# Kernel tuning notes

Measured on AMD Instinct MI355X. Metric: run time of the kernel, lower is better.

## Reference

```python
import jax, jax.numpy as jnp
import numpy as np

CODE_NUM = 100000
GRAPH = 256
HIDDEN = 256
TIME = 256


def gru_cell(x, h, w_ih, w_hh, b_ih, b_hh):
    # torch.nn.GRUCell math. x:[N,G] h:[N,H] w_ih:[3H,G] w_hh:[3H,H]
    gi = x @ w_ih.T + b_ih
    gh = h @ w_hh.T + b_hh
    i_r, i_z, i_n = jnp.split(gi, 3, axis=-1)
    h_r, h_z, h_n = jnp.split(gh, 3, axis=-1)
    r = jax.nn.sigmoid(i_r + h_r)
    z = jax.nn.sigmoid(i_z + h_z)
    n = jnp.tanh(i_n + r * h_n)
    return (1.0 - z) * n + z * h


def setup_inputs() -> dict:
    key = jax.random.key(0)
    ks = jax.random.split(key, 12)
    s_ih = 1.0 / np.sqrt(HIDDEN)
    return {
        "interval": jax.random.uniform(ks[0], (1,), jnp.float32) * 100.0 + 1.0,
        "t": 0,
        "co_embeddings": jax.random.normal(ks[1], (CODE_NUM, GRAPH), jnp.float32),
        "divided": jax.random.randint(ks[2], (CODE_NUM, 3), 0, 2, jnp.int32),
        "no_embeddings": jax.random.normal(ks[3], (1, GRAPH), jnp.float32),
        "unrelated_embeddings": jax.random.normal(ks[4], (1, GRAPH), jnp.float32),
        "is_last": 0,
        "hidden_state": jax.random.normal(ks[5], (CODE_NUM, HIDDEN), jnp.float32),
        "weight_ih": jax.random.uniform(ks[6], (3 * HIDDEN, GRAPH), jnp.float32, -s_ih, s_ih),
        "weight_hh": jax.random.uniform(ks[7], (3 * HIDDEN, HIDDEN), jnp.float32, -s_ih, s_ih),
        "bias_ih": jax.random.uniform(ks[8], (3 * HIDDEN,), jnp.float32, -s_ih, s_ih),
        "bias_hh": jax.random.uniform(ks[9], (3 * HIDDEN,), jnp.float32, -s_ih, s_ih),
        "time_w": jax.random.normal(ks[10], (TIME, 1), jnp.float32) * 0.02,
        "time_b": jax.random.normal(ks[11], (TIME,), jnp.float32) * 0.02,
    }


def reference(interval, t, co_embeddings, divided, no_embeddings,
              unrelated_embeddings, is_last, hidden_state,
              weight_ih, weight_hh, bias_ih, bias_hh, time_w, time_b):
    # time branch: tanh(Linear(1/log(interval + e)))
    inv = 1.0 / jnp.log(interval[:, None] + jnp.exp(jnp.float32(1.0)))  # [1,1]
    time_features = jnp.tanh(inv @ time_w.T + time_b)                  # [1,TIME]

    # not is_last branch: gather rows where any of divided[:,0:3] > 0,
    # run GRUCell, scatter into zeros, max-reduce over selected rows.
    # Masked formulation is row-wise exact (GRUCell acts per row).
    mask = jnp.any(divided > 0, axis=1)                                 # [N]
    h_all = gru_cell(co_embeddings, hidden_state,
                     weight_ih, weight_hh, bias_ih, bias_hh)            # [N,H]
    h_new = jnp.where(mask[:, None], h_all, 0.0)                        # scatter into zeros
    output = jnp.max(jnp.where(mask[:, None], h_all, -jnp.inf), axis=0) # max over gathered rows, [H]
    return output + time_features, h_new
```

## Files before the change

kernel.cpp:

```cpp
#include <hip/hip_runtime.h>
#include <hip/hip_bf16.h>
#include <math.h>

#define M_ROWS 100000
#define NGROUPS 3125
#define NTILES_TOTAL 391
#define TILES_PER_XCD 49
#define ROWS_PER_XCD 12500
#define NTILES 49
#define NCHUNK 49152

typedef __attribute__((ext_vector_type(8)))  short  short8;
typedef __attribute__((ext_vector_type(16))) float  float16v;

__device__ __forceinline__ unsigned short bf16_rne(float f) {
    unsigned u = __builtin_bit_cast(unsigned, f);
    u += 0x7FFFu + ((u >> 16) & 1u);
    return (unsigned short)(u >> 16);
}

__device__ __forceinline__ float sigmoid_fast(float x) {
    return 1.0f / (1.0f + __expf(-x));
}
__device__ __forceinline__ float tanh_fast(float x) {
    return 1.0f - 2.0f / (__expf(2.0f * x) + 1.0f);
}

__device__ __forceinline__ unsigned pack2_rn(float lo, float hi) {
    __hip_bfloat162 t = __float22bfloat162_rn(float2{lo, hi});
    unsigned u;
    __builtin_memcpy(&u, &t, 4);
    return u;
}

__device__ __forceinline__ short8 pack_bf16x8(float4 a, float4 b) {
    union { short8 s; unsigned u[4]; } r;
    r.u[0] = pack2_rn(a.x, a.y);
    r.u[1] = pack2_rn(a.z, a.w);
    r.u[2] = pack2_rn(b.x, b.y);
    r.u[3] = pack2_rn(b.z, b.w);
    return r.s;
}

__global__ void prep_kernel(const float* __restrict__ X,
                            const float* __restrict__ H,
                            const float* __restrict__ wih,
                            const float* __restrict__ whh,
                            const int* __restrict__ divided,
                            unsigned short* __restrict__ wswz,
                            unsigned short* __restrict__ apack,
                            unsigned int* __restrict__ maxacc,
                            int* __restrict__ maskbuf,
                            unsigned int* __restrict__ donecnt,
                            int pack_blocks)
{
    const int b   = blockIdx.x;
    const int tid = threadIdx.x;

    if (b < pack_blocks) {
        int gt   = b * 256 + tid;
        int lane = gt & 63;
        int u    = gt >> 6;
        int gr   = u >> 4;
        int kc   = u & 15;
        int row  = gr * 32 + (lane & 31);
        int col  = kc * 16 + (lane >> 5) * 8;
        const float* xs = X + (size_t)row * 256 + col;
        const float* hs = H + (size_t)row * 256 + col;
        float4 a = reinterpret_cast<const float4*>(xs)[0];
        float4 c = reinterpret_cast<const float4*>(xs)[1];
        reinterpret_cast<short8*>(apack)[(size_t)(u * 2) * 64 + lane] = pack_bf16x8(a, c);
        float4 d = reinterpret_cast<const float4*>(hs)[0];
        float4 e = reinterpret_cast<const float4*>(hs)[1];
        reinterpret_cast<short8*>(apack)[(size_t)(u * 2 + 1) * 64 + lane] = pack_bf16x8(d, e);
        return;
    }

    int bb = b - pack_blocks;
    if (bb < 192) {
        int idx  = bb * 256 + tid;
        int lane = idx & 63;
        int t    = idx >> 6;
        int s    = t % 6;
        int t2   = t / 6;
        int kc   = t2 & 15;
        int g    = t2 >> 4;
        int row  = (s % 3) * 256 + g * 32 + (lane & 31);
        int col  = kc * 16 + (lane >> 5) * 8;
        const float* src = (s < 3 ? wih : whh) + row * 256 + col;
        float4 a = reinterpret_cast<const float4*>(src)[0];
        float4 c = reinterpret_cast<const float4*>(src)[1];
        uint4 p;
        p.x = (unsigned)bf16_rne(a.x) | ((unsigned)bf16_rne(a.y) << 16);
        p.y = (unsigned)bf16_rne(a.z) | ((unsigned)bf16_rne(a.w) << 16);
        p.z = (unsigned)bf16_rne(c.x) | ((unsigned)bf16_rne(c.y) << 16);
        p.w = (unsigned)bf16_rne(c.z) | ((unsigned)bf16_rne(c.w) << 16);
        reinterpret_cast<uint4*>(wswz)[idx] = p;
    } else if (bb < 192 + 391) {
        int m = (bb - 192) * 256 + tid;
        if (m < M_ROWS)
            maskbuf[m] = (divided[3 * m] > 0) | (divided[3 * m + 1] > 0) | (divided[3 * m + 2] > 0);
    } else {
        maxacc[tid] = 0u;
        if (tid == 0) *donecnt = 0u;
    }
}

__global__ __launch_bounds__(512, 2) void gru_main_packed(
    const unsigned short* __restrict__ Apack,
    const float* __restrict__ H,
    const unsigned short* __restrict__ Wswz,
    const float* __restrict__ bih,
    const float* __restrict__ bhh,
    const int* __restrict__ maskbuf,
    const float* __restrict__ interval,
    const float* __restrict__ time_w,
    const float* __restrict__ time_b,
    float* __restrict__ hnew,
    unsigned int* __restrict__ maxacc,
    unsigned int* __restrict__ donecnt,
    float* __restrict__ out)
{
    __shared__ unsigned short Wlds[49152];
    __shared__ int islast;

    const int tid  = threadIdx.x;
    const int lane = tid & 63;
    const int wave = tid >> 6;
    const int l32  = lane & 31;
    const int hi   = lane >> 5;

    const int b    = blockIdx.x;
    const int xcd  = b & 7;
    const int slot = b >> 3;
    const int g    = slot & 7;
    const int sub  = slot >> 3;

    const int tbeg = xcd * TILES_PER_XCD + sub;
    const int tend = min(xcd * TILES_PER_XCD + TILES_PER_XCD, NTILES_TOTAL);

    {
        const uint4* ws = reinterpret_cast<const uint4*>(Wswz) + (size_t)g * 6144;
        uint4* wd = reinterpret_cast<uint4*>(Wlds);
        #pragma unroll
        for (int i = 0; i < 12; ++i) wd[i * 512 + tid] = ws[i * 512 + tid];
    }
    __syncthreads();

    const short8* wbase = reinterpret_cast<const short8*>(Wlds);
    const short8* A8b   = reinterpret_cast<const short8*>(Apack);
    const int jj = g * 32 + l32;
    const float bir = bih[jj], biz = bih[256 + jj], bin_ = bih[512 + jj];
    const float bhr = bhh[jj], bhz = bhh[256 + jj], bhn  = bhh[512 + jj];

    float colmax = -__builtin_inff();

    for (int t = tbeg; t < tend; t += 4) {
        const int wrow0 = t * 256 + wave * 32;
        if (wrow0 >= M_ROWS) continue;
        const int gr0 = wrow0 >> 5;
        const short8* A8 = A8b + (size_t)gr0 * 2048 + lane;

        float16v acc[6];
        #pragma unroll
        for (int s = 0; s < 6; ++s)
            #pragma unroll
            for (int q = 0; q < 16; ++q) acc[s][q] = 0.0f;

        short8 bx[4], bh[4];
        #pragma unroll
        for (int p = 0; p < 4; ++p) {
            bx[p] = A8[p * 128];
            bh[p] = A8[p * 128 + 64];
        }

        #pragma unroll
        for (int kc = 0; kc < 16; ++kc) {
            const int cur = kc & 3;
            const short8 ax = bx[cur];
            const short8 ah = bh[cur];
            if (kc < 12) {
                bx[cur] = A8[(kc + 4) * 128];
                bh[cur] = A8[(kc + 4) * 128 + 64];
            }
            const short8* wk = wbase + kc * 384 + lane;
            acc[0] = __builtin_amdgcn_mfma_f32_32x32x16_bf16(ax, wk[0],   acc[0], 0, 0, 0);
            acc[1] = __builtin_amdgcn_mfma_f32_32x32x16_bf16(ax, wk[64],  acc[1], 0, 0, 0);
            acc[2] = __builtin_amdgcn_mfma_f32_32x32x16_bf16(ax, wk[128], acc[2], 0, 0, 0);
            acc[3] = __builtin_amdgcn_mfma_f32_32x32x16_bf16(ah, wk[192], acc[3], 0, 0, 0);
            acc[4] = __builtin_amdgcn_mfma_f32_32x32x16_bf16(ah, wk[256], acc[4], 0, 0, 0);
            acc[5] = __builtin_amdgcn_mfma_f32_32x32x16_bf16(ah, wk[320], acc[5], 0, 0, 0);
        }

        #pragma unroll
        for (int reg = 0; reg < 16; ++reg) {
            const int rl = (reg & 3) + 8 * (reg >> 2) + 4 * hi;
            const int m  = wrow0 + rl;
            float gir = acc[0][reg] + bir;
            float giz = acc[1][reg] + biz;
            float gin = acc[2][reg] + bin_;
            float ghr = acc[3][reg] + bhr;
            float ghz = acc[4][reg] + bhz;
            float ghn = acc[5][reg] + bhn;
            float r = sigmoid_fast(gir + ghr);
            float z = sigmoid_fast(giz + ghz);
            float n = tanh_fast(gin + r * ghn);
            float hp = H[(size_t)m * 256 + jj];
            float hv = (1.0f - z) * n + z * hp;
            int mk = maskbuf[m];
            __builtin_nontemporal_store(mk ? hv : 0.0f, &hnew[(size_t)m * 256 + jj]);
            if (mk) colmax = fmaxf(colmax, hv);
        }
    }

    colmax = fmaxf(colmax, __shfl_xor(colmax, 32));
    if (hi == 0) {
        unsigned bb = __builtin_bit_cast(unsigned, colmax);
        unsigned u  = (bb & 0x80000000u) ? ~bb : (bb | 0x80000000u);
        atomicMax(&maxacc[jj], u);
    }

    __syncthreads();
    if (tid == 0) {
        __threadfence();
        islast = (atomicAdd(donecnt, 1u) == 255u) ? 1 : 0;
    }
    __syncthreads();
    if (islast && tid < 256) {
        unsigned u  = atomicMax(&maxacc[tid], 0u);
        unsigned bb2 = (u & 0x80000000u) ? (u & 0x7FFFFFFFu) : ~u;
        float mx  = __builtin_bit_cast(float, bb2);
        float inv = 1.0f / logf(interval[0] + 2.718281828459045f);
        out[tid]  = mx + tanhf(inv * time_w[tid] + time_b[tid]);
    }
}

__global__ __launch_bounds__(512, 2) void gru_main_legacy(
    const float* __restrict__ X,
    const float* __restrict__ H,
    const unsigned short* __restrict__ Wswz,
    const float* __restrict__ bih,
    const float* __restrict__ bhh,
    const int* __restrict__ maskbuf,
    float* __restrict__ hnew,
    unsigned int* __restrict__ maxacc)
{
    __shared__ unsigned short Wlds[NCHUNK];

    const int tid  = threadIdx.x;
    const int lane = tid & 63;
    const int wave = tid >> 6;
    const int l32  = lane & 31;
    const int hi   = lane >> 5;

    const int b    = blockIdx.x;
    const int xcd  = b & 7;
    const int slot = b >> 3;
    const int g    = slot & 7;
    const int sub  = slot >> 3;
    const int base  = xcd * ROWS_PER_XCD;
    const int limit = base + ROWS_PER_XCD;

    {
        const uint4* ws = reinterpret_cast<const uint4*>(Wswz) + (size_t)g * 6144;
        uint4* wd = reinterpret_cast<uint4*>(Wlds);
        #pragma unroll
        for (int i = 0; i < 12; ++i) wd[i * 512 + tid] = ws[i * 512 + tid];
    }
    __syncthreads();

    const short8* wbase = reinterpret_cast<const short8*>(Wlds);
    const int jj = g * 32 + l32;
    const float bir = bih[jj], biz = bih[256 + jj], bin_ = bih[512 + jj];
    const float bhr = bhh[jj], bhz = bhh[256 + jj], bhn  = bhh[512 + jj];

    float colmax = -__builtin_inff();

    for (int t = sub; t < NTILES; t += 4) {
        const int wrow0 = base + t * 256 + wave * 32;
        if (wrow0 >= limit) continue;
        const int arow = min(wrow0 + l32, limit - 1);
        const float4* X4 = reinterpret_cast<const float4*>(X) + (size_t)arow * 64;
        const float4* H4 = reinterpret_cast<const float4*>(H) + (size_t)arow * 64;

        float16v acc[6];
        #pragma unroll
        for (int s = 0; s < 6; ++s)
            #pragma unroll
            for (int q = 0; q < 16; ++q) acc[s][q] = 0.0f;

        float4 xb[2][4], hb[2][4];
        #pragma unroll
        for (int c = 0; c < 2; ++c)
            #pragma unroll
            for (int f = 0; f < 2; ++f) {
                int fi = c * 4 + hi * 2 + f;
                xb[0][c * 2 + f] = X4[fi];
                hb[0][c * 2 + f] = H4[fi];
            }

        #pragma unroll
        for (int q = 0; q < 8; ++q) {
            const int cur = q & 1, nxt = cur ^ 1;
            if (q < 7) {
                #pragma unroll
                for (int c = 0; c < 2; ++c)
                    #pragma unroll
                    for (int f = 0; f < 2; ++f) {
                        int fi = (q * 2 + 2 + c) * 4 + hi * 2 + f;
                        xb[nxt][c * 2 + f] = X4[fi];
                        hb[nxt][c * 2 + f] = H4[fi];
                    }
            }
            short8 ax[2], ah[2];
            #pragma unroll
            for (int c = 0; c < 2; ++c) {
                ax[c] = pack_bf16x8(xb[cur][c * 2], xb[cur][c * 2 + 1]);
                ah[c] = pack_bf16x8(hb[cur][c * 2], hb[cur][c * 2 + 1]);
            }
            #pragma unroll
            for (int c = 0; c < 2; ++c) {
                const int kc = q * 2 + c;
                const short8* wk = wbase + (kc * 6) * 64 + lane;
                acc[0] = __builtin_amdgcn_mfma_f32_32x32x16_bf16(ax[c], wk[0],   acc[0], 0, 0, 0);
                acc[1] = __builtin_amdgcn_mfma_f32_32x32x16_bf16(ax[c], wk[64],  acc[1], 0, 0, 0);
                acc[2] = __builtin_amdgcn_mfma_f32_32x32x16_bf16(ax[c], wk[128], acc[2], 0, 0, 0);
                acc[3] = __builtin_amdgcn_mfma_f32_32x32x16_bf16(ah[c], wk[192], acc[3], 0, 0, 0);
                acc[4] = __builtin_amdgcn_mfma_f32_32x32x16_bf16(ah[c], wk[256], acc[4], 0, 0, 0);
                acc[5] = __builtin_amdgcn_mfma_f32_32x32x16_bf16(ah[c], wk[320], acc[5], 0, 0, 0);
            }
        }

        #pragma unroll
        for (int reg = 0; reg < 16; ++reg) {
            int rl = (reg & 3) + 8 * (reg >> 2) + 4 * hi;
            int m  = wrow0 + rl;
            if (m < limit) {
                float gir = acc[0][reg] + bir;
                float giz = acc[1][reg] + biz;
                float gin = acc[2][reg] + bin_;
                float ghr = acc[3][reg] + bhr;
                float ghz = acc[4][reg] + bhz;
                float ghn = acc[5][reg] + bhn;
                float r = sigmoid_fast(gir + ghr);
                float z = sigmoid_fast(giz + ghz);
                float n = tanh_fast(gin + r * ghn);
                float hp = H[(size_t)m * 256 + jj];
                float hv = (1.0f - z) * n + z * hp;
                int mk = maskbuf[m];
                __builtin_nontemporal_store(mk ? hv : 0.0f, &hnew[(size_t)m * 256 + jj]);
                if (mk) colmax = fmaxf(colmax, hv);
            }
        }
    }

    colmax = fmaxf(colmax, __shfl_xor(colmax, 32));
    if (hi == 0) {
        unsigned bb = __builtin_bit_cast(unsigned, colmax);
        unsigned u  = (bb & 0x80000000u) ? ~bb : (bb | 0x80000000u);
        atomicMax(&maxacc[jj], u);
    }
}

__global__ void finalize_kernel(const unsigned int* __restrict__ maxacc,
                                const float* __restrict__ interval,
                                const float* __restrict__ time_w,
                                const float* __restrict__ time_b,
                                float* __restrict__ out)
{
    int j = threadIdx.x;
    unsigned u = maxacc[j];
    unsigned b = (u & 0x80000000u) ? (u & 0x7FFFFFFFu) : ~u;
    float mx = __builtin_bit_cast(float, b);
    float inv = 1.0f / logf(interval[0] + 2.718281828459045f);
    out[j] = mx + tanhf(inv * time_w[j] + time_b[j]);
}

extern "C" void kernel_launch(void* const* d_in, const int* in_sizes, int n_in,
                              void* d_out, int out_size, void* d_ws, size_t ws_size,
                              hipStream_t stream) {
    const float* interval = (const float*)d_in[0];
    const float* co       = (const float*)d_in[2];
    const int*   divided  = (const int*)d_in[3];
    const float* hidden   = (const float*)d_in[7];
    const float* wih      = (const float*)d_in[8];
    const float* whh      = (const float*)d_in[9];
    const float* bih      = (const float*)d_in[10];
    const float* bhh      = (const float*)d_in[11];
    const float* time_w   = (const float*)d_in[12];
    const float* time_b   = (const float*)d_in[13];

    float* out  = (float*)d_out;
    float* hnew = out + 256;

    unsigned short* wswz    = (unsigned short*)d_ws;
    unsigned int*   maxacc  = (unsigned int*)((char*)d_ws + 786432);
    int*            maskbuf = (int*)((char*)d_ws + 787456);
    unsigned int*   donecnt = (unsigned int*)((char*)d_ws + 1187456);
    unsigned short* apack   = (unsigned short*)((char*)d_ws + 2097152);

    const size_t NEED = 2097152ull + 102400000ull;
    const bool packed = (ws_size >= NEED);
    const int pb = packed ? 12500 : 0;

    prep_kernel<<<pb + 584, 256, 0, stream>>>(co, hidden, wih, whh, divided,
                                              wswz, apack, maxacc, maskbuf,
                                              donecnt, pb);

    if (packed) {
        gru_main_packed<<<256, 512, 0, stream>>>(apack, hidden, wswz, bih, bhh,
                                                 maskbuf, interval, time_w, time_b,
                                                 hnew, maxacc, donecnt, out);
    } else {
        gru_main_legacy<<<256, 512, 0, stream>>>(co, hidden, wswz,
                                                 bih, bhh, maskbuf, hnew, maxacc);
        finalize_kernel<<<1, 256, 0, stream>>>(maxacc, interval, time_w, time_b, out);
    }
}
```

Before: 459.0 us.

## Process two row groups per wave with register-cached weights and cross-tile prefetch

Each wave now computes two 32-row groups per iteration, so each weight fragment loaded from LDS feeds two MFMAs. Weight fragments are double-buffered in registers, and A-operand loads for the next tile are prefetched during the current tile's K loop. Work is split into 512-row super-tiles balanced across XCDs. The aim is to halve LDS weight traffic per MFMA and hide global load latency between tiles. The cost is many more accumulator and operand registers, which can lower occupancy or cause spills.

Result: slower. 522.2 us (+13.8%).

```diff
diff --git a/kernel.cpp b/kernel.cpp
--- a/kernel.cpp
+++ b/kernel.cpp
@@ -4,8 +4,7 @@
 
 #define M_ROWS 100000
 #define NGROUPS 3125
-#define NTILES_TOTAL 391
-#define TILES_PER_XCD 49
+#define NSUPER 196
 #define ROWS_PER_XCD 12500
 #define NTILES 49
 #define NCHUNK 49152
@@ -136,8 +135,8 @@
     const int g    = slot & 7;
     const int sub  = slot >> 3;
 
-    const int tbeg = xcd * TILES_PER_XCD + sub;
-    const int tend = min(xcd * TILES_PER_XCD + TILES_PER_XCD, NTILES_TOTAL);
+    const int sbeg = xcd * 24 + (xcd < 4 ? xcd : 4);
+    const int send = sbeg + (xcd < 4 ? 25 : 24);
 
     {
         const uint4* ws = reinterpret_cast<const uint4*>(Wswz) + (size_t)g * 6144;
@@ -155,61 +154,105 @@
 
     float colmax = -__builtin_inff();
 
-    for (int t = tbeg; t < tend; t += 4) {
-        const int wrow0 = t * 256 + wave * 32;
-        if (wrow0 >= M_ROWS) continue;
-        const int gr0 = wrow0 >> 5;
-        const short8* A8 = A8b + (size_t)gr0 * 2048 + lane;
-
-        float16v acc[6];
-        #pragma unroll
-        for (int s = 0; s < 6; ++s)
+    short8 wr[2][6];
+    #pragma unroll
+    for (int s = 0; s < 6; ++s) wr[0][s] = wbase[s * 64 + lane];
+
+    short8 bx0[4], bh0[4], bx1[4], bh1[4];
+    const int T0 = sbeg + sub;
+    {
+        int gp0 = T0 * 16 + 2 * wave; if (gp0 > NGROUPS - 1) gp0 = NGROUPS - 1;
+        int gp1 = gp0 + 1;            if (gp1 > NGROUPS - 1) gp1 = NGROUPS - 1;
+        const short8* P0 = A8b + (size_t)gp0 * 2048 + lane;
+        const short8* P1 = A8b + (size_t)gp1 * 2048 + lane;
+        #pragma unroll
+        for (int p = 0; p < 4; ++p) {
+            bx0[p] = P0[p * 128]; bh0[p] = P0[p * 128 + 64];
+            bx1[p] = P1[p * 128]; bh1[p] = P1[p * 128 + 64];
+        }
+    }
+
+    for (int T = T0; T < send; T += 4) {
+        const int gr0 = T * 16 + 2 * wave;
+        if (gr0 >= NGROUPS) continue;
+        const int gr1 = gr0 + 1;
+        const bool v1 = (gr1 < NGROUPS);
+
+        const short8* A0c = A8b + (size_t)gr0 * 2048 + lane;
+        const short8* A1c = A8b + (size_t)(v1 ? gr1 : gr0) * 2048 + lane;
+
+        int Tn = T + 4; if (Tn >= send) Tn = T;
+        int ng0 = Tn * 16 + 2 * wave; if (ng0 >= NGROUPS) ng0 = gr0;
+        int ng1 = ng0 + 1;            if (ng1 >= NGROUPS) ng1 = ng0;
+        const short8* A0n = A8b + (size_t)ng0 * 2048 + lane;
+        const short8* A1n = A8b + (size_t)ng1 * 2048 + lane;
+
+        float16v acc[12];
+        #pragma unroll
+        for (int s = 0; s < 12; ++s)
             #pragma unroll
             for (int q = 0; q < 16; ++q) acc[s][q] = 0.0f;
 
-        short8 bx[4], bh[4];
-        #pragma unroll
-        for (int p = 0; p < 4; ++p) {
-            bx[p] = A8[p * 128];
-            bh[p] = A8[p * 128 + 64];
+        #pragma unroll
+        for (int kc = 0; kc < 16; ++kc) {
+            const int sl = kc & 3;
+            const short8 ax0 = bx0[sl], ah0 = bh0[sl];
+            const short8 ax1 = bx1[sl], ah1 = bh1[sl];
+
+            {
+                const int kr = kc + 4;
+                const short8* P0 = (kr < 16) ? A0c : A0n;
+                const short8* P1 = (kr < 16) ? A1c : A1n;
+                const int ko = (kr < 16) ? kr : (kr - 16);
+                bx0[sl] = P0[ko * 128]; bh0[sl] = P0[ko * 128 + 64];
+                bx1[sl] = P1[ko * 128]; bh1[sl] = P1[ko * 128 + 64];
+            }
+
+            const int cb = kc & 1;
+            {
+                const int kn = (kc + 1) & 15;
+                const short8* wn = wbase + kn * 384 + lane;
+                #pragma unroll
+                for (int s = 0; s < 6; ++s) wr[cb ^ 1][s] = wn[s * 64];
+            }
+
+            acc[0]  = __builtin_amdgcn_mfma_f32_32x32x16_bf16(ax0, wr[cb][0], acc[0],  0, 0, 0);
+            acc[6]  = __builtin_amdgcn_mfma_f32_32x32x16_bf16(ax1, wr[cb][0], acc[6],  0, 0, 0);
+            acc[1]  = __builtin_amdgcn_mfma_f32_32x32x16_bf16(ax0, wr[cb][1], acc[1],  0, 0, 0);
+            acc[7]  = __builtin_amdgcn_mfma_f32_32x32x16_bf16(ax1, wr[cb][1], acc[7],  0, 0, 0);
+            acc[2]  = __builtin_amdgcn_mfma_f32_32x32x16_bf16(ax0, wr[cb][2], acc[2],  0, 0, 0);
+            acc[8]  = __builtin_amdgcn_mfma_f32_32x32x16_bf16(ax1, wr[cb][2], acc[8],  0, 0, 0);
+            acc[3]  = __builtin_amdgcn_mfma_f32_32x32x16_bf16(ah0, wr[cb][3], acc[3],  0, 0, 0);
+            acc[9]  = __builtin_amdgcn_mfma_f32_32x32x16_bf16(ah1, wr[cb][3], acc[9],  0, 0, 0);
+            acc[4]  = __builtin_amdgcn_mfma_f32_32x32x16_bf16(ah0, wr[cb][4], acc[4],  0, 0, 0);
+            acc[10] = __builtin_amdgcn_mfma_f32_32x32x16_bf16(ah1, wr[cb][4], acc[10], 0, 0, 0);
+            acc[5]  = __builtin_amdgcn_mfma_f32_32x32x16_bf16(ah0, wr[cb][5], acc[5],  0, 0, 0);
+            acc[11] = __builtin_amdgcn_mfma_f32_32x32x16_bf16(ah1, wr[cb][5], acc[11], 0, 0, 0);
         }
 
         #pragma unroll
-        for (int kc = 0; kc < 16; ++kc) {
-            const int cur = kc & 3;
-            const short8 ax = bx[cur];
-            const short8 ah = bh[cur];
-            if (kc < 12) {
-                bx[cur] = A8[(kc + 4) * 128];
-                bh[cur] = A8[(kc + 4) * 128 + 64];
-            }
-            const short8* wk = wbase + kc * 384 + lane;
-            acc[0] = __builtin_amdgcn_mfma_f32_32x32x16_bf16(ax, wk[0],   acc[0], 0, 0, 0);
-            acc[1] = __builtin_amdgcn_mfma_f32_32x32x16_bf16(ax, wk[64],  acc[1], 0, 0, 0);
-            acc[2] = __builtin_amdgcn_mfma_f32_32x32x16_bf16(ax, wk[128], acc[2], 0, 0, 0);
-            acc[3] = __builtin_amdgcn_mfma_f32_32x32x16_bf16(ah, wk[192], acc[3], 0, 0, 0);
-            acc[4] = __builtin_amdgcn_mfma_f32_32x32x16_bf16(ah, wk[256], acc[4], 0, 0, 0);
-            acc[5] = __builtin_amdgcn_mfma_f32_32x32x16_bf16(ah, wk[320], acc[5], 0, 0, 0);
-        }
-
-        #pragma unroll
-        for (int reg = 0; reg < 16; ++reg) {
-            const int rl = (reg & 3) + 8 * (reg >> 2) + 4 * hi;
-            const int m  = wrow0 + rl;
-            float gir = acc[0][reg] + bir;
-            float giz = acc[1][reg] + biz;
-            float gin = acc[2][reg] + bin_;
-            float ghr = acc[3][reg] + bhr;
-            float ghz = acc[4][reg] + bhz;
-            float ghn = acc[5][reg] + bhn;
-            float r = sigmoid_fast(gir + ghr);
-            float z = sigmoid_fast(giz + ghz);
-            float n = tanh_fast(gin + r * ghn);
-            float hp = H[(size_t)m * 256 + jj];
-            float hv = (1.0f - z) * n + z * hp;
-            int mk = maskbuf[m];
-            __builtin_nontemporal_store(mk ? hv : 0.0f, &hnew[(size_t)m * 256 + jj]);
-            if (mk) colmax = fmaxf(colmax, hv);
+        for (int grp = 0; grp < 2; ++grp) {
+            if (grp == 1 && !v1) continue;
+            const int mb = (grp ? gr1 : gr0) * 32;
+            #pragma unroll
+            for (int reg = 0; reg < 16; ++reg) {
+                const int rl = (reg & 3) + 8 * (reg >> 2) + 4 * hi;
+                const int m  = mb + rl;
+                float gir = acc[grp * 6 + 0][reg] + bir;
+                float giz = acc[grp * 6 + 1][reg] + biz;
+                float gin = acc[grp * 6 + 2][reg] + bin_;
+                float ghr = acc[grp * 6 + 3][reg] + bhr;
+                float ghz = acc[grp * 6 + 4][reg] + bhz;
+                float ghn = acc[grp * 6 + 5][reg] + bhn;
+                float r = sigmoid_fast(gir + ghr);
+                float z = sigmoid_fast(giz + ghz);
+                float n = tanh_fast(gin + r * ghn);
+                float hp = H[(size_t)m * 256 + jj];
+                float hv = (1.0f - z) * n + z * hp;
+                int mk = maskbuf[m];
+                __builtin_nontemporal_store(mk ? hv : 0.0f, &hnew[(size_t)m * 256 + jj]);
+                if (mk) colmax = fmaxf(colmax, hv);
+            }
         }
     }
 
```

## Switch packed GRU path to 16x16x32 MFMA tiles with LDS-staged packing

Applied to the files above, without the earlier changes.

Changes the packed path from 32x32x16 to 16x16x32 bf16 MFMA. Weights are split into 16 column groups and the launch becomes 768 blocks of 256 threads, each wave looping over 16-row groups. The A operand for the next group is prefetched across iterations, and H and mask values are loaded before the matmul. The activation pack kernel now stages 32 rows through LDS so global reads and writes are coalesced. This targets occupancy, latency hiding and pack-kernel efficiency, at the cost of smaller MFMA tiles and three times as many blocks contending on the completion counter.

New measurement: 766.7 us. 67.0% more time.

```diff
diff --git a/kernel.cpp b/kernel.cpp
--- a/kernel.cpp
+++ b/kernel.cpp
@@ -3,14 +3,13 @@
 #include <math.h>
 
 #define M_ROWS 100000
-#define NGROUPS 3125
-#define NTILES_TOTAL 391
-#define TILES_PER_XCD 49
+#define NG16 6250
 #define ROWS_PER_XCD 12500
 #define NTILES 49
 #define NCHUNK 49152
 
 typedef __attribute__((ext_vector_type(8)))  short  short8;
+typedef __attribute__((ext_vector_type(4)))  float  float4v;
 typedef __attribute__((ext_vector_type(16))) float  float16v;
 
 __device__ __forceinline__ unsigned short bf16_rne(float f) {
@@ -52,27 +51,41 @@
                             unsigned int* __restrict__ maxacc,
                             int* __restrict__ maskbuf,
                             unsigned int* __restrict__ donecnt,
-                            int pack_blocks)
+                            int pack_blocks, int w16)
 {
+    __shared__ unsigned short slds[2][32][264];
+
     const int b   = blockIdx.x;
     const int tid = threadIdx.x;
 
     if (b < pack_blocks) {
-        int gt   = b * 256 + tid;
-        int lane = gt & 63;
-        int u    = gt >> 6;
-        int gr   = u >> 4;
-        int kc   = u & 15;
-        int row  = gr * 32 + (lane & 31);
-        int col  = kc * 16 + (lane >> 5) * 8;
-        const float* xs = X + (size_t)row * 256 + col;
-        const float* hs = H + (size_t)row * 256 + col;
-        float4 a = reinterpret_cast<const float4*>(xs)[0];
-        float4 c = reinterpret_cast<const float4*>(xs)[1];
-        reinterpret_cast<short8*>(apack)[(size_t)(u * 2) * 64 + lane] = pack_bf16x8(a, c);
-        float4 d = reinterpret_cast<const float4*>(hs)[0];
-        float4 e = reinterpret_cast<const float4*>(hs)[1];
-        reinterpret_cast<short8*>(apack)[(size_t)(u * 2 + 1) * 64 + lane] = pack_bf16x8(d, e);
+        const int r0 = b * 32;
+        #pragma unroll
+        for (int it = 0; it < 16; ++it) {
+            const int mat = it >> 3;
+            const int idx = (it & 7) * 256 + tid;
+            const int row = idx >> 6;
+            const int c4  = idx & 63;
+            const float* sp = (mat ? H : X) + (size_t)(r0 + row) * 256 + c4 * 4;
+            float4 v = *reinterpret_cast<const float4*>(sp);
+            uint2 w;
+            w.x = pack2_rn(v.x, v.y);
+            w.y = pack2_rn(v.z, v.w);
+            *reinterpret_cast<uint2*>(&slds[mat][row][c4 * 4]) = w;
+        }
+        __syncthreads();
+        #pragma unroll
+        for (int it = 0; it < 8; ++it) {
+            const int o    = it * 256 + tid;
+            const int gl   = o >> 10;
+            const int kc   = (o >> 7) & 7;
+            const int mat  = (o >> 6) & 1;
+            const int lane = o & 63;
+            const int rl   = gl * 16 + (lane & 15);
+            const int col  = kc * 32 + (lane >> 4) * 8;
+            short8 v = *reinterpret_cast<const short8*>(&slds[mat][rl][col]);
+            reinterpret_cast<short8*>(apack)[(size_t)b * 2048 + o] = v;
+        }
         return;
     }
 
@@ -83,11 +96,19 @@
         int t    = idx >> 6;
         int s    = t % 6;
         int t2   = t / 6;
-        int kc   = t2 & 15;
-        int g    = t2 >> 4;
-        int row  = (s % 3) * 256 + g * 32 + (lane & 31);
-        int col  = kc * 16 + (lane >> 5) * 8;
-        const float* src = (s < 3 ? wih : whh) + row * 256 + col;
+        int row, col;
+        if (w16) {
+            int kc  = t2 & 7;
+            int g16 = t2 >> 3;
+            row = (s % 3) * 256 + g16 * 16 + (lane & 15);
+            col = kc * 32 + (lane >> 4) * 8;
+        } else {
+            int kc = t2 & 15;
+            int g  = t2 >> 4;
+            row = (s % 3) * 256 + g * 32 + (lane & 31);
+            col = kc * 16 + (lane >> 5) * 8;
+        }
+        const float* src = (s < 3 ? wih : whh) + (size_t)row * 256 + col;
         float4 a = reinterpret_cast<const float4*>(src)[0];
         float4 c = reinterpret_cast<const float4*>(src)[1];
         uint4 p;
@@ -106,7 +127,7 @@
     }
 }
 
-__global__ __launch_bounds__(512, 2) void gru_main_packed(
+__global__ __launch_bounds__(256, 3) void gru_main16(
     const unsigned short* __restrict__ Apack,
     const float* __restrict__ H,
     const unsigned short* __restrict__ Wswz,
@@ -121,113 +142,116 @@
     unsigned int* __restrict__ donecnt,
     float* __restrict__ out)
 {
-    __shared__ unsigned short Wlds[49152];
+    __shared__ unsigned short Wlds[24576];
     __shared__ int islast;
 
     const int tid  = threadIdx.x;
     const int lane = tid & 63;
     const int wave = tid >> 6;
-    const int l32  = lane & 31;
-    const int hi   = lane >> 5;
+    const int l16  = lane & 15;
+    const int q    = lane >> 4;
 
     const int b    = blockIdx.x;
     const int xcd  = b & 7;
     const int slot = b >> 3;
-    const int g    = slot & 7;
-    const int sub  = slot >> 3;
-
-    const int tbeg = xcd * TILES_PER_XCD + sub;
-    const int tend = min(xcd * TILES_PER_XCD + TILES_PER_XCD, NTILES_TOTAL);
+    const int g16  = slot & 15;
+    const int sub  = slot >> 4;
+
+    const int gbeg = xcd * 781 + (xcd < 2 ? xcd : 2);
+    const int gend = gbeg + 781 + (xcd < 2 ? 1 : 0);
 
     {
-        const uint4* ws = reinterpret_cast<const uint4*>(Wswz) + (size_t)g * 6144;
+        const uint4* ws = reinterpret_cast<const uint4*>(Wswz) + (size_t)g16 * 3072;
         uint4* wd = reinterpret_cast<uint4*>(Wlds);
         #pragma unroll
-        for (int i = 0; i < 12; ++i) wd[i * 512 + tid] = ws[i * 512 + tid];
+        for (int i = 0; i < 12; ++i) wd[i * 256 + tid] = ws[i * 256 + tid];
     }
     __syncthreads();
 
     const short8* wbase = reinterpret_cast<const short8*>(Wlds);
     const short8* A8b   = reinterpret_cast<const short8*>(Apack);
-    const int jj = g * 32 + l32;
+    const int jj = g16 * 16 + l16;
     const float bir = bih[jj], biz = bih[256 + jj], bin_ = bih[512 + jj];
     const float bhr = bhh[jj], bhz = bhh[256 + jj], bhn  = bhh[512 + jj];
 
     float colmax = -__builtin_inff();
 
-    for (int t = tbeg; t < tend; t += 4) {
-        const int wrow0 = t * 256 + wave * 32;
-        if (wrow0 >= M_ROWS) continue;
-        const int gr0 = wrow0 >> 5;
-        const short8* A8 = A8b + (size_t)gr0 * 2048 + lane;
-
-        float16v acc[6];
-        #pragma unroll
-        for (int s = 0; s < 6; ++s)
-            #pragma unroll
-            for (int q = 0; q < 16; ++q) acc[s][q] = 0.0f;
-
+    int g0 = gbeg + sub * 4 + wave;
+    if (g0 < gend) {
+        const short8* A8 = A8b + (size_t)g0 * 1024 + lane;
         short8 bx[4], bh[4];
         #pragma unroll
-        for (int p = 0; p < 4; ++p) {
-            bx[p] = A8[p * 128];
-            bh[p] = A8[p * 128 + 64];
-        }
-
-        #pragma unroll
-        for (int kc = 0; kc < 16; ++kc) {
-            const int cur = kc & 3;
-            const short8 ax = bx[cur];
-            const short8 ah = bh[cur];
-            if (kc < 12) {
-                bx[cur] = A8[(kc + 4) * 128];
-                bh[cur] = A8[(kc + 4) * 128 + 64];
-            }
-            const short8* wk = wbase + kc * 384 + lane;
-            acc[0] = __builtin_amdgcn_mfma_f32_32x32x16_bf16(ax, wk[0],   acc[0], 0, 0, 0);
-            acc[1] = __builtin_amdgcn_mfma_f32_32x32x16_bf16(ax, wk[64],  acc[1], 0, 0, 0);
-            acc[2] = __builtin_amdgcn_mfma_f32_32x32x16_bf16(ax, wk[128], acc[2], 0, 0, 0);
-            acc[3] = __builtin_amdgcn_mfma_f32_32x32x16_bf16(ah, wk[192], acc[3], 0, 0, 0);
-            acc[4] = __builtin_amdgcn_mfma_f32_32x32x16_bf16(ah, wk[256], acc[4], 0, 0, 0);
-            acc[5] = __builtin_amdgcn_mfma_f32_32x32x16_bf16(ah, wk[320], acc[5], 0, 0, 0);
-        }
-
-        #pragma unroll
-        for (int reg = 0; reg < 16; ++reg) {
-            const int rl = (reg & 3) + 8 * (reg >> 2) + 4 * hi;
-            const int m  = wrow0 + rl;
-            float gir = acc[0][reg] + bir;
-            float giz = acc[1][reg] + biz;
-            float gin = acc[2][reg] + bin_;
-            float ghr = acc[3][reg] + bhr;
-            float ghz = acc[4][reg] + bhz;
-            float ghn = acc[5][reg] + bhn;
-            float r = sigmoid_fast(gir + ghr);
-            float z = sigmoid_fast(giz + ghz);
-            float n = tanh_fast(gin + r * ghn);
-            float hp = H[(size_t)m * 256 + jj];
-            float hv = (1.0f - z) * n + z * hp;
-            int mk = maskbuf[m];
-            __builtin_nontemporal_store(mk ? hv : 0.0f, &hnew[(size_t)m * 256 + jj]);
-            if (mk) colmax = fmaxf(colmax, hv);
-        }
-    }
-
+        for (int p = 0; p < 4; ++p) { bx[p] = A8[p * 128]; bh[p] = A8[p * 128 + 64]; }
+
+        for (int g = g0; g < gend; g += 24) {
+            A8 = A8b + (size_t)g * 1024 + lane;
+            int gn = g + 24; if (gn >= gend) gn = g;
+            const short8* An = A8b + (size_t)gn * 1024 + lane;
+
+            float hp[4]; int mk[4];
+            #pragma unroll
+            for (int r = 0; r < 4; ++r) {
+                const int m = g * 16 + q * 4 + r;
+                hp[r] = H[(size_t)m * 256 + jj];
+                mk[r] = maskbuf[m];
+            }
+
+            float4v acc[6];
+            #pragma unroll
+            for (int s = 0; s < 6; ++s)
+                #pragma unroll
+                for (int r = 0; r < 4; ++r) acc[s][r] = 0.0f;
+
+            #pragma unroll
+            for (int kc = 0; kc < 8; ++kc) {
+                const int sl = kc & 3;
+                const short8 ax = bx[sl], ah = bh[sl];
+                if (kc < 4) { bx[sl] = A8[(kc + 4) * 128]; bh[sl] = A8[(kc + 4) * 128 + 64]; }
+                else        { bx[sl] = An[(kc - 4) * 128]; bh[sl] = An[(kc - 4) * 128 + 64]; }
+                const short8* wk = wbase + kc * 384 + lane;
+                acc[0] = __builtin_amdgcn_mfma_f32_16x16x32_bf16(ax, wk[0],   acc[0], 0, 0, 0);
+                acc[1] = __builtin_amdgcn_mfma_f32_16x16x32_bf16(ax, wk[64],  acc[1], 0, 0, 0);
+                acc[2] = __builtin_amdgcn_mfma_f32_16x16x32_bf16(ax, wk[128], acc[2], 0, 0, 0);
+                acc[3] = __builtin_amdgcn_mfma_f32_16x16x32_bf16(ah, wk[192], acc[3], 0, 0, 0);
+                acc[4] = __builtin_amdgcn_mfma_f32_16x16x32_bf16(ah, wk[256], acc[4], 0, 0, 0);
+                acc[5] = __builtin_amdgcn_mfma_f32_16x16x32_bf16(ah, wk[320], acc[5], 0, 0, 0);
+            }
+
+            #pragma unroll
+            for (int r = 0; r < 4; ++r) {
+                const int m = g * 16 + q * 4 + r;
+                float gir = acc[0][r] + bir;
+                float giz = acc[1][r] + biz;
+                float gin = acc[2][r] + bin_;
+                float ghr = acc[3][r] + bhr;
+                float ghz = acc[4][r] + bhz;
+                float ghn = acc[5][r] + bhn;
+                float rr = sigmoid_fast(gir + ghr);
+                float z  = sigmoid_fast(giz + ghz);
+                float n  = tanh_fast(gin + rr * ghn);
+                float hv = (1.0f - z) * n + z * hp[r];
+                __builtin_nontemporal_store(mk[r] ? hv : 0.0f, &hnew[(size_t)m * 256 + jj]);
+                if (mk[r]) colmax = fmaxf(colmax, hv);
+            }
+        }
+    }
+
+    colmax = fmaxf(colmax, __shfl_xor(colmax, 16));
     colmax = fmaxf(colmax, __shfl_xor(colmax, 32));
-    if (hi == 0) {
-        unsigned bb = __builtin_bit_cast(unsigned, colmax);
-        unsigned u  = (bb & 0x80000000u) ? ~bb : (bb | 0x80000000u);
+    if (lane < 16) {
+        unsigned bb2 = __builtin_bit_cast(unsigned, colmax);
+        unsigned u   = (bb2 & 0x80000000u) ? ~bb2 : (bb2 | 0x80000000u);
         atomicMax(&maxacc[jj], u);
     }
 
     __syncthreads();
     if (tid == 0) {
         __threadfence();
-        islast = (atomicAdd(donecnt, 1u) == 255u) ? 1 : 0;
+        islast = (atomicAdd(donecnt, 1u) == 767u) ? 1 : 0;
     }
     __syncthreads();
-    if (islast && tid < 256) {
-        unsigned u  = atomicMax(&maxacc[tid], 0u);
+    if (islast) {
+        unsigned u   = ((volatile unsigned int*)maxacc)[tid];
         unsigned bb2 = (u & 0x80000000u) ? (u & 0x7FFFFFFFu) : ~u;
         float mx  = __builtin_bit_cast(float, bb2);
         float inv = 1.0f / logf(interval[0] + 2.718281828459045f);
@@ -287,7 +311,7 @@
         #pragma unroll
         for (int s = 0; s < 6; ++s)
             #pragma unroll
-            for (int q = 0; q < 16; ++q) acc[s][q] = 0.0f;
+            for (int qq = 0; qq < 16; ++qq) acc[s][qq] = 0.0f;
 
         float4 xb[2][4], hb[2][4];
         #pragma unroll
@@ -300,14 +324,14 @@
             }
 
         #pragma unroll
-        for (int q = 0; q < 8; ++q) {
-            const int cur = q & 1, nxt = cur ^ 1;
-            if (q < 7) {
+        for (int qq = 0; qq < 8; ++qq) {
+            const int cur = qq & 1, nxt = cur ^ 1;
+            if (qq < 7) {
                 #pragma unroll
                 for (int c = 0; c < 2; ++c)
                     #pragma unroll
                     for (int f = 0; f < 2; ++f) {
-                        int fi = (q * 2 + 2 + c) * 4 + hi * 2 + f;
+                        int fi = (qq * 2 + 2 + c) * 4 + hi * 2 + f;
                         xb[nxt][c * 2 + f] = X4[fi];
                         hb[nxt][c * 2 + f] = H4[fi];
                     }
@@ -320,7 +344,7 @@
             }
             #pragma unroll
             for (int c = 0; c < 2; ++c) {
-                const int kc = q * 2 + c;
+                const int kc = qq * 2 + c;
                 const short8* wk = wbase + (kc * 6) * 64 + lane;
                 acc[0] = __builtin_amdgcn_mfma_f32_32x32x16_bf16(ax[c], wk[0],   acc[0], 0, 0, 0);
                 acc[1] = __builtin_amdgcn_mfma_f32_32x32x16_bf16(ax[c], wk[64],  acc[1], 0, 0, 0);
@@ -345,19 +369,19 @@
                 float r = sigmoid_fast(gir + ghr);
                 float z = sigmoid_fast(giz + ghz);
                 float n = tanh_fast(gin + r * ghn);
-                float hp = H[(size_t)m * 256 + jj];
-                float hv = (1.0f - z) * n + z * hp;
-                int mk = maskbuf[m];
-                __builtin_nontemporal_store(mk ? hv : 0.0f, &hnew[(size_t)m * 256 + jj]);
-                if (mk) colmax = fmaxf(colmax, hv);
+                float hpv = H[(size_t)m * 256 + jj];
+                float hv = (1.0f - z) * n + z * hpv;
+                int mkk = maskbuf[m];
+                __builtin_nontemporal_store(mkk ? hv : 0.0f, &hnew[(size_t)m * 256 + jj]);
+                if (mkk) colmax = fmaxf(colmax, hv);
             }
         }
     }
 
     colmax = fmaxf(colmax, __shfl_xor(colmax, 32));
     if (hi == 0) {
-        unsigned bb = __builtin_bit_cast(unsigned, colmax);
-        unsigned u  = (bb & 0x80000000u) ? ~bb : (bb | 0x80000000u);
+        unsigned bb2 = __builtin_bit_cast(unsigned, colmax);
+        unsigned u  = (bb2 & 0x80000000u) ? ~bb2 : (bb2 | 0x80000000u);
         atomicMax(&maxacc[jj], u);
     }
 }
@@ -401,16 +425,16 @@
 
     const size_t NEED = 2097152ull + 102400000ull;
     const bool packed = (ws_size >= NEED);
-    const int pb = packed ? 12500 : 0;
+    const int pb = packed ? 3125 : 0;
 
     prep_kernel<<<pb + 584, 256, 0, stream>>>(co, hidden, wih, whh, divided,
                                               wswz, apack, maxacc, maskbuf,
-                                              donecnt, pb);
+                                              donecnt, pb, packed ? 1 : 0);
 
     if (packed) {
-        gru_main_packed<<<256, 512, 0, stream>>>(apack, hidden, wswz, bih, bhh,
-                                                 maskbuf, interval, time_w, time_b,
-                                                 hnew, maxacc, donecnt, out);
+        gru_main16<<<768, 256, 0, stream>>>(apack, hidden, wswz, bih, bhh,
+                                            maskbuf, interval, time_w, time_b,
+                                            hnew, maxacc, donecnt, out);
     } else {
         gru_main_legacy<<<256, 512, 0, stream>>>(co, hidden, wswz,
                                                  bih, bhh, maskbuf, hnew, maxacc);
```
